# Performance work log

Hardware: AMD Instinct MI355X
Metric: run time of the kernel (lower is better)

The kernel has to match this reference:

```python
import jax, jax.numpy as jnp
import numpy as np
from jax import lax

N, C, M = 512, 81, 28
NMS_THRESH = 0.5
EPS = 1e-4


def setup_inputs() -> dict:
    key = jax.random.key(0)
    k1, k2, k3, k4 = jax.random.split(key, 4)
    return {
        "left_logits": jax.random.normal(k1, (N, C, M, M), dtype=jnp.float32),
        "right_logits": jax.random.normal(k2, (N, C, M, M), dtype=jnp.float32),
        "scores": jax.random.uniform(k3, (N,), dtype=jnp.float32),
        "labels": jax.random.randint(k4, (N,), 0, C),
    }


def mask_nms_keep(probs, scores, thresh):
    # probs: [N, M, M] float mask probabilities; greedy suppression in score order.
    n = probs.shape[0]
    order = jnp.argsort(-scores)
    P = probs[order].reshape(n, -1)                  # [N, M*M] sorted by score desc
    inter = P @ P.T                                   # pairwise sum(mask_i * mask_j)
    u = P.sum(-1)                                     # per-mask area (numerator mask only)
    iou = inter / (u[:, None] + EPS)                  # asymmetric IoU as in mask_iou()
    upper = jnp.triu(jnp.ones((n, n), dtype=bool), 1) # j > i

    def body(i, suppressed):
        sup_row = (~suppressed[i]) & upper[i] & (iou[i] >= thresh)
        return suppressed | sup_row

    suppressed = lax.fori_loop(0, n, body, jnp.zeros(n, dtype=bool))
    keep_sorted = ~suppressed
    # map back to original detection order
    return jnp.zeros(n, dtype=bool).at[order].set(keep_sorted)


def reference(left_logits, right_logits, scores, labels):
    idx = jnp.arange(left_logits.shape[0])
    # full-tensor sigmoid then per-class gather, as in the original module
    left_prob = jax.nn.sigmoid(left_logits)[idx, labels][:, None]    # [N,1,M,M]
    right_prob = jax.nn.sigmoid(right_logits)[idx, labels][:, None]  # [N,1,M,M]

    # filter_empty: both sides must have nonzero mask mass
    valid = (left_prob[:, 0].sum((-1, -2)) > 0) & (right_prob[:, 0].sum((-1, -2)) > 0)

    left_keep = mask_nms_keep(left_prob[:, 0], scores, NMS_THRESH)
    right_keep = mask_nms_keep(right_prob[:, 0], scores, NMS_THRESH)
    keep = valid & left_keep & right_keep  # intersection of left/right NMS keeps

    probs = jnp.stack([left_prob, right_prob], axis=0)  # [2,N,1,M,M]
    return probs, keep
```

## Files before the change

kernel.cpp:

```cpp
#include <hip/hip_runtime.h>
#include <math.h>

#define NDET 512
#define NCLS 81
#define MM   784
#define PROBS_ELEMS (2 * NDET * MM)
#define NMS_TH 0.5
#define EPS_D  1e-4
#define SDD 114


__global__ __launch_bounds__(256) void k12_fused(
    const float* __restrict__ left, const float* __restrict__ right,
    const float* __restrict__ scores, const int* __restrict__ labels,
    float* __restrict__ out, double* __restrict__ u, int* __restrict__ order) {
  if (blockIdx.x == 256) {
    __shared__ float sk[NDET];
    __shared__ int   si[NDET];
    int t = threadIdx.x;
    for (int e = t; e < NDET; e += 256) { sk[e] = scores[e]; si[e] = e; }
    __syncthreads();
    for (int k = 2; k <= NDET; k <<= 1) {
      for (int j = k >> 1; j > 0; j >>= 1) {
        for (int e = t; e < NDET; e += 256) {
          int p = e ^ j;
          if (p > e) {
            bool dir = ((e & k) == 0);
            float sa = sk[e], sb = sk[p];
            int ia = si[e], ib = si[p];
            bool aBeforeB = (sa > sb) || (sa == sb && ia < ib);
            bool doSwap = dir ? (!aBeforeB) : aBeforeB;
            if (doSwap) { sk[e] = sb; si[e] = ib; sk[p] = sa; si[p] = ia; }
          }
        }
        __syncthreads();
      }
    }
    for (int e = t; e < NDET; e += 256) order[e] = si[e];
    return;
  }

  int wv = threadIdx.x >> 6;
  int lane = threadIdx.x & 63;
  int m = (blockIdx.x << 2) | wv;
  int s = m >> 9;
  int n = m & 511;
  const float* src = (s == 0) ? left : right;
  int lab = labels[n];
  const float4* in4 = (const float4*)(src + ((size_t)n * NCLS + lab) * MM);
  float4* out4 = (float4*)(out + ((size_t)s * NDET + n) * MM);
  double local = 0.0;
  for (int i = lane; i < MM / 4; i += 64) {
    float4 v = in4[i];
    float4 r;
    r.x = 1.0f / (1.0f + expf(-v.x));
    r.y = 1.0f / (1.0f + expf(-v.y));
    r.z = 1.0f / (1.0f + expf(-v.z));
    r.w = 1.0f / (1.0f + expf(-v.w));
    out4[i] = r;
    local += (double)r.x + (double)r.y + (double)r.z + (double)r.w;
  }
#pragma unroll
  for (int off = 32; off > 0; off >>= 1)
    local += __shfl_down(local, off, 64);
  if (lane == 0) u[s * NDET + n] = local;
}

__global__ __launch_bounds__(256) void k3_iou(
    const float* __restrict__ P,
    const double* __restrict__ u,
    const int* __restrict__ order,
    unsigned int* __restrict__ bits32) {
  int bi = blockIdx.x;
  int s = bi / 136;
  int tri = bi % 136;
  int ti = 0, rem = tri;
  while (rem >= 16 - ti) { rem -= 16 - ti; ti++; }
  int tj = ti + rem;

  __shared__ __align__(16) double Asd[32][SDD];
  __shared__ __align__(16) double Bsd[32][SDD];
  __shared__ double Cp[3][32][33];
  __shared__ int oi[32], oj[32];
  __shared__ double den05[32];
  __shared__ unsigned char pred[32][32];

  int t = threadIdx.x;
  if (t < 32) {
    int r = order[ti * 32 + t];
    oi[t] = r;
    den05[t] = 0.5 * (u[s * NDET + r] + EPS_D);
    oj[t] = order[tj * 32 + t];
  }
  __syncthreads();

  const float* Pside = P + (size_t)s * NDET * MM;

  const float4* gsrc[7];
  double* ldst[7];
#pragma unroll
  for (int i = 0; i < 7; i++) {
    int idx = t + 256 * i;
    int ab = (idx >= 896);
    int idc = ab ? (idx - 896) : idx;
    int r = idc / 28;
    int c4 = idc - r * 28;
    int o = ab ? oj[r] : oi[r];
    gsrc[i] = (const float4*)(Pside + (size_t)o * MM) + c4;
    ldst[i] = ab ? &Bsd[r][4 * c4] : &Asd[r][4 * c4];
  }

  float4 pf[7];
#pragma unroll
  for (int i = 0; i < 7; i++) pf[i] = gsrc[i][0];

  int wv = t >> 6;
  int lane = t & 63;
  int tx = lane & 7;
  int ty = (lane >> 3) & 7;
  int kb = 28 * wv;

  double acc[4][4];
#pragma unroll
  for (int i = 0; i < 4; i++)
#pragma unroll
    for (int j = 0; j < 4; j++) acc[i][j] = 0.0;

  for (int kc = 0; kc < 7; kc++) {
#pragma unroll
    for (int i = 0; i < 7; i++) {
      float4 v = pf[i];
      double2 d0; d0.x = (double)v.x; d0.y = (double)v.y;
      double2 d1; d1.x = (double)v.z; d1.y = (double)v.w;
      *(double2*)(ldst[i])     = d0;
      *(double2*)(ldst[i] + 2) = d1;
    }
    __syncthreads();
    if (kc < 6) {
#pragma unroll
      for (int i = 0; i < 7; i++) pf[i] = gsrc[i][(kc + 1) * 28];
    }
#pragma unroll
    for (int kp = 0; kp < 14; kp++) {
      double2 av[4], bv[4];
#pragma unroll
      for (int i = 0; i < 4; i++)
        av[i] = *(const double2*)&Asd[ty + 8 * i][kb + 2 * kp];
#pragma unroll
      for (int j = 0; j < 4; j++)
        bv[j] = *(const double2*)&Bsd[tx + 8 * j][kb + 2 * kp];
#pragma unroll
      for (int i = 0; i < 4; i++)
#pragma unroll
        for (int j = 0; j < 4; j++) {
          acc[i][j] = fma(av[i].x, bv[j].x, acc[i][j]);
          acc[i][j] = fma(av[i].y, bv[j].y, acc[i][j]);
        }
    }
    __syncthreads();
  }

  if (wv > 0) {
#pragma unroll
    for (int i = 0; i < 4; i++)
#pragma unroll
      for (int j = 0; j < 4; j++)
        Cp[wv - 1][ty + 8 * i][tx + 8 * j] = acc[i][j];
  }
  __syncthreads();
  if (wv == 0) {
#pragma unroll
    for (int i = 0; i < 4; i++) {
      int r = ty + 8 * i;
#pragma unroll
      for (int j = 0; j < 4; j++) {
        int c = tx + 8 * j;
        double v = acc[i][j] + Cp[0][r][c] + Cp[1][r][c] + Cp[2][r][c];
        pred[r][c] = (v >= den05[r]) ? 1 : 0;
      }
    }
  }
  __syncthreads();
  if (t < 32) {
    unsigned m = 0;
#pragma unroll
    for (int c = 0; c < 32; c++) m |= ((unsigned)pred[t][c]) << c;
    bits32[((size_t)s * NDET + ti * 32 + t) * 16 + tj] = m;
  }
}

__global__ __launch_bounds__(512) void k4_greedy(
    const unsigned long long* __restrict__ bits,
    const int* __restrict__ order,
    const double* __restrict__ u,
    float* __restrict__ outKeep) {
  __shared__ unsigned long long B[2 * NDET * 8];
  __shared__ unsigned char keepO[2 * NDET];
  int t = threadIdx.x;

  for (int e = t; e < 2 * NDET * 8; e += 512) {
    unsigned long long w = bits[e];
    int g = e & 7;
    int i = (e >> 3) & 511;
    int gi = i >> 6;
    if (g < gi) {
      w = 0ull;
    } else if (g == gi) {
      int li = i & 63;
      w = (li == 63) ? 0ull : (w & (~0ull << (li + 1)));
    }
    B[e] = w;
  }
  __syncthreads();

  int wv = t >> 6;
  int lane = t & 63;
  if (wv < 2) {
    int s = wv;
    const unsigned long long* Bside = B + (size_t)s * NDET * 8;
    unsigned long long S0 = 0, S1 = 0, S2 = 0, S3 = 0,
                       S4 = 0, S5 = 0, S6 = 0, S7 = 0;

#define GROUP(G, SG, ORS)                                              \
    for (int li = 0; li < 64; li++) {                                  \
      unsigned act = (unsigned)((SG >> li) & 1ull);                    \
      if (__builtin_amdgcn_readfirstlane(act) == 0) {                  \
        const unsigned long long* row = Bside + ((((G) << 6) | li) << 3); \
        ORS                                                            \
      }                                                                \
    }
    GROUP(0, S0, { S0 |= row[0]; S1 |= row[1]; S2 |= row[2]; S3 |= row[3];
                   S4 |= row[4]; S5 |= row[5]; S6 |= row[6]; S7 |= row[7]; })
    GROUP(1, S1, { S1 |= row[1]; S2 |= row[2]; S3 |= row[3];
                   S4 |= row[4]; S5 |= row[5]; S6 |= row[6]; S7 |= row[7]; })
    GROUP(2, S2, { S2 |= row[2]; S3 |= row[3];
                   S4 |= row[4]; S5 |= row[5]; S6 |= row[6]; S7 |= row[7]; })
    GROUP(3, S3, { S3 |= row[3];
                   S4 |= row[4]; S5 |= row[5]; S6 |= row[6]; S7 |= row[7]; })
    GROUP(4, S4, { S4 |= row[4]; S5 |= row[5]; S6 |= row[6]; S7 |= row[7]; })
    GROUP(5, S5, { S5 |= row[5]; S6 |= row[6]; S7 |= row[7]; })
    GROUP(6, S6, { S6 |= row[6]; S7 |= row[7]; })
    GROUP(7, S7, { S7 |= row[7]; })
#undef GROUP

    unsigned long long Sarr[8] = {S0, S1, S2, S3, S4, S5, S6, S7};
#pragma unroll
    for (int g = 0; g < 8; g++) {
      int c = (g << 6) | lane;
      keepO[s * NDET + order[c]] =
          (unsigned char)(((Sarr[g] >> lane) & 1ull) ^ 1ull);
    }
  }
  __syncthreads();

  if (t < NDET) {
    bool valid = (u[t] > 0.0) && (u[NDET + t] > 0.0);
    outKeep[t] = (valid && keepO[t] && keepO[NDET + t]) ? 1.0f : 0.0f;
  }
}

extern "C" void kernel_launch(void* const* d_in, const int* in_sizes, int n_in,
                              void* d_out, int out_size, void* d_ws, size_t ws_size,
                              hipStream_t stream) {
  const float* left   = (const float*)d_in[0];
  const float* right  = (const float*)d_in[1];
  const float* scores = (const float*)d_in[2];
  const int*   labels = (const int*)d_in[3];
  float* out = (float*)d_out;

  char* ws = (char*)d_ws;
  double* u                = (double*)(ws + 0);
  int* order               = (int*)(ws + 8192);
  unsigned int* bits32     = (unsigned int*)(ws + 16384);
  unsigned long long* bits = (unsigned long long*)(ws + 16384);

  k12_fused<<<257, 256, 0, stream>>>(left, right, scores, labels, out, u, order);
  k3_iou<<<272, 256, 0, stream>>>(out, u, order, bits32);
  k4_greedy<<<1, 512, 0, stream>>>(bits, order, u, out + PROBS_ELEMS);
}
```

Before: 285.9 us.

## Double IoU block to 512 threads with 8-way split-K and aliased shared arena

The pairwise IoU tile kernel now runs 8 wavefronts per block instead of 4, each handling 14 of the 112 K columns per chunk, and the partial sums of 7 waves are reduced by wave 0. Shared memory for the A/B tiles and the partial-sum buffer is aliased into one arena so the larger reduction buffer fits. This aims to raise latency hiding in a kernel that only has 272 blocks, but it adds a longer serial reduction and uses non-unrolled, runtime-bounded loops for the loads.

```diff
diff --git a/kernel.cpp b/kernel.cpp
--- a/kernel.cpp
+++ b/kernel.cpp
@@ -66,7 +66,7 @@
   if (lane == 0) u[s * NDET + n] = local;
 }
 
-__global__ __launch_bounds__(256) void k3_iou(
+__global__ __launch_bounds__(512, 4) void k3_iou(
     const float* __restrict__ P,
     const double* __restrict__ u,
     const int* __restrict__ order,
@@ -78,9 +78,10 @@
   while (rem >= 16 - ti) { rem -= 16 - ti; ti++; }
   int tj = ti + rem;
 
-  __shared__ __align__(16) double Asd[32][SDD];
-  __shared__ __align__(16) double Bsd[32][SDD];
-  __shared__ double Cp[3][32][33];
+  __shared__ __align__(16) double arena[7 * 32 * 33];
+  double (*Asd)[SDD] = (double (*)[SDD])arena;
+  double (*Bsd)[SDD] = (double (*)[SDD])(arena + 32 * SDD);
+  double (*Cp)[33]   = (double (*)[33])arena;
   __shared__ int oi[32], oj[32];
   __shared__ double den05[32];
   __shared__ unsigned char pred[32][32];
@@ -96,29 +97,34 @@
 
   const float* Pside = P + (size_t)s * NDET * MM;
 
-  const float4* gsrc[7];
-  double* ldst[7];
-#pragma unroll
-  for (int i = 0; i < 7; i++) {
-    int idx = t + 256 * i;
-    int ab = (idx >= 896);
-    int idc = ab ? (idx - 896) : idx;
-    int r = idc / 28;
-    int c4 = idc - r * 28;
-    int o = ab ? oj[r] : oi[r];
-    gsrc[i] = (const float4*)(Pside + (size_t)o * MM) + c4;
-    ldst[i] = ab ? &Bsd[r][4 * c4] : &Asd[r][4 * c4];
-  }
-
-  float4 pf[7];
-#pragma unroll
-  for (int i = 0; i < 7; i++) pf[i] = gsrc[i][0];
+  const float4* gsrc[4];
+  double* ldst[4];
+  int nslot = (t < 256) ? 4 : 3;
+#pragma unroll
+  for (int i = 0; i < 4; i++) {
+    int idx = t + 512 * i;
+    if (idx < 1792) {
+      int ab = (idx >= 896);
+      int idc = ab ? (idx - 896) : idx;
+      int r = idc / 28;
+      int c4 = idc - r * 28;
+      int o = ab ? oj[r] : oi[r];
+      gsrc[i] = (const float4*)(Pside + (size_t)o * MM) + c4;
+      ldst[i] = ab ? &Bsd[r][4 * c4] : &Asd[r][4 * c4];
+    } else {
+      gsrc[i] = (const float4*)(Pside);
+      ldst[i] = &Asd[0][0];
+    }
+  }
+
+  float4 pf[4];
+  for (int i = 0; i < nslot; i++) pf[i] = gsrc[i][0];
 
   int wv = t >> 6;
   int lane = t & 63;
   int tx = lane & 7;
-  int ty = (lane >> 3) & 7;
-  int kb = 28 * wv;
+  int ty = lane >> 3;
+  int kb = 14 * wv;
 
   double acc[4][4];
 #pragma unroll
@@ -127,8 +133,7 @@
     for (int j = 0; j < 4; j++) acc[i][j] = 0.0;
 
   for (int kc = 0; kc < 7; kc++) {
-#pragma unroll
-    for (int i = 0; i < 7; i++) {
+    for (int i = 0; i < nslot; i++) {
       float4 v = pf[i];
       double2 d0; d0.x = (double)v.x; d0.y = (double)v.y;
       double2 d1; d1.x = (double)v.z; d1.y = (double)v.w;
@@ -137,11 +142,10 @@
     }
     __syncthreads();
     if (kc < 6) {
-#pragma unroll
-      for (int i = 0; i < 7; i++) pf[i] = gsrc[i][(kc + 1) * 28];
-    }
-#pragma unroll
-    for (int kp = 0; kp < 14; kp++) {
+      for (int i = 0; i < nslot; i++) pf[i] = gsrc[i][(kc + 1) * 28];
+    }
+#pragma unroll
+    for (int kp = 0; kp < 7; kp++) {
       double2 av[4], bv[4];
 #pragma unroll
       for (int i = 0; i < 4; i++)
@@ -165,7 +169,7 @@
     for (int i = 0; i < 4; i++)
 #pragma unroll
       for (int j = 0; j < 4; j++)
-        Cp[wv - 1][ty + 8 * i][tx + 8 * j] = acc[i][j];
+        Cp[(wv - 1) * 32 + ty + 8 * i][tx + 8 * j] = acc[i][j];
   }
   __syncthreads();
   if (wv == 0) {
@@ -175,7 +179,9 @@
 #pragma unroll
       for (int j = 0; j < 4; j++) {
         int c = tx + 8 * j;
-        double v = acc[i][j] + Cp[0][r][c] + Cp[1][r][c] + Cp[2][r][c];
+        double v = acc[i][j];
+#pragma unroll
+        for (int p = 0; p < 7; p++) v += Cp[p * 32 + r][c];
         pred[r][c] = (v >= den05[r]) ? 1 : 0;
       }
     }
@@ -275,6 +281,6 @@
   unsigned long long* bits = (unsigned long long*)(ws + 16384);
 
   k12_fused<<<257, 256, 0, stream>>>(left, right, scores, labels, out, u, order);
-  k3_iou<<<272, 256, 0, stream>>>(out, u, order, bits32);
+  k3_iou<<<272, 512, 0, stream>>>(out, u, order, bits32);
   k4_greedy<<<1, 512, 0, stream>>>(bits, order, u, out + PROBS_ELEMS);
 }
```

After: 300.6 us. 1.05x slower.
